# Kernel optimization log

Measured on AMD Instinct MI355X. Metric: run time of the kernel, lower is better.

The kernel has to match this reference:

```python
import jax, jax.numpy as jnp
import numpy as np


def setup_inputs() -> dict:
    key = jax.random.key(0)
    k1, k2, k3, k4, k5 = jax.random.split(key, 5)
    B, C, V, D, O = 8, 64, 25000, 12, 64
    x = jax.random.normal(k1, (B, C, V), dtype=jnp.float32)
    nbr_idx = jax.random.randint(k2, (B, V, D), 0, V, dtype=jnp.int32)
    # true 1-ring valence in [1, D]
    deg = jax.random.randint(k3, (B, V), 1, D + 1, dtype=jnp.int32)
    # conv weight [O, C, 1, 2] flattened to [O, C, 2], fan-in init scale
    W = jax.random.normal(k4, (O, C, 2), dtype=jnp.float32) * (1.0 / np.sqrt(C * 2))
    b = jax.random.normal(k5, (O,), dtype=jnp.float32) * 0.01
    return {"x": x, "nbr_idx": nbr_idx, "deg": deg, "W": W, "b": b}


def reference(x, nbr_idx, deg, W, b):
    # x: [B, C, V]; nbr_idx: [B, V, D] padded 1-ring; deg: [B, V] valid count
    B, C, V = x.shape
    D = nbr_idx.shape[-1]
    # gather neighbor features: [B, C, V, D]
    gathered = jax.vmap(lambda xb, ib: xb[:, ib])(x, nbr_idx)
    mask = (jnp.arange(D, dtype=deg.dtype)[None, None, :] < deg[:, :, None])  # [B, V, D]
    maskf = mask.astype(x.dtype)[:, None, :, :]  # [B, 1, V, D]
    denom = jnp.maximum(deg, 1).astype(x.dtype)[:, None, :]  # [B, 1, V]
    nbr_mean = jnp.sum(gathered * maskf, axis=-1) / denom  # [B, C, V]
    # G: [B, C, V, 2] = (self feature, 1-ring mean); conv2d kernel (1,2)
    G = jnp.stack([x, nbr_mean], axis=-1)
    out = jnp.einsum('bcvk,ock->bov', G, W) + b[None, :, None]
    return out[..., None]  # [B, O, V, 1]
```

## Files before the change

kernel.cpp:

```cpp
#include <hip/hip_runtime.h>
#include <stdint.h>


#define NB 8
#define NC 64
#define NV 25000
#define ND 12
#define NO 64
#define VT 98
#define GT 391

typedef uint32_t u32x4 __attribute__((ext_vector_type(4)));
typedef uint32_t u32x2 __attribute__((ext_vector_type(2)));
typedef __bf16  bf16x8 __attribute__((ext_vector_type(8)));
typedef float   f32x4  __attribute__((ext_vector_type(4)));

__device__ inline uint32_t bf16pack(float a, float b) {
    uint32_t ua = __float_as_uint(a), ub = __float_as_uint(b);
    ua = (ua + 0x7fffu + ((ua >> 16) & 1u)) >> 16;
    ub = (ub + 0x7fffu + ((ub >> 16) & 1u)) >> 16;
    return ua | (ub << 16);
}
__device__ inline float blo(uint32_t u) { return __uint_as_float(u << 16); }
__device__ inline float bhi(uint32_t u) { return __uint_as_float(u & 0xffff0000u); }

__global__ __launch_bounds__(256) void wt_kernel(const float* __restrict__ W,
                                                 uint32_t* __restrict__ Wcb) {
    int i = blockIdx.x * 256 + threadIdx.x;
    int m = i >> 5;
    int c = (i & 31) * 2;
    int k = m >> 6;
    int o = m & 63;
    float s0 = W[o * (NC * 2) + c * 2 + k];
    float s1 = W[o * (NC * 2) + (c + 1) * 2 + k];
    Wcb[i] = bf16pack(s0, s1);
}

__global__ __launch_bounds__(256) void ygemm_mfma(const float* __restrict__ x,
                                                  const uint32_t* __restrict__ Wcb,
                                                  const float* __restrict__ bias,
                                                  uint32_t* __restrict__ y0,
                                                  uint32_t* __restrict__ y1) {
    const int b = blockIdx.x & 7;
    const int tile = blockIdx.x >> 3;
    const int wave = threadIdx.x >> 6;
    const int lane = threadIdx.x & 63;
    const int l15 = lane & 15;
    const int lq = lane >> 4;
    const int v = tile * 64 + wave * 16 + l15;
    const int vc = v < NV ? v : NV - 1;
    const float* xb = x + (size_t)b * NC * NV;

    union BU { uint32_t u[4]; bf16x8 v; } bu[2];
#pragma unroll
    for (int kt = 0; kt < 2; ++kt) {
        const float* xc = xb + (size_t)(kt * 32 + lq * 8) * NV + vc;
#pragma unroll
        for (int jp = 0; jp < 4; ++jp) {
            float s0 = __builtin_nontemporal_load(xc + (size_t)(2 * jp) * NV);
            float s1 = __builtin_nontemporal_load(xc + (size_t)(2 * jp + 1) * NV);
            bu[kt].u[jp] = bf16pack(s0, s1);
        }
    }

    f32x4 acc[8];
#pragma unroll
    for (int mt = 0; mt < 8; ++mt) acc[mt] = (f32x4){0.f, 0.f, 0.f, 0.f};

#pragma unroll
    for (int mt = 0; mt < 8; ++mt) {
#pragma unroll
        for (int kt = 0; kt < 2; ++kt) {
            union { u32x4 q; bf16x8 v; } au;
            au.q = *(const u32x4*)(Wcb + (size_t)(mt * 16 + l15) * 32 + kt * 16 + lq * 4);
            acc[mt] = __builtin_amdgcn_mfma_f32_16x16x32_bf16(au.v, bu[kt].v, acc[mt], 0, 0, 0);
        }
    }

    if (v < NV) {
        uint32_t* yr0 = y0 + ((size_t)b * NV + v) * 32;
        uint32_t* yr1 = y1 + ((size_t)b * NV + v) * 32;
#pragma unroll
        for (int mt = 0; mt < 8; ++mt) {
            const int mo = mt * 16 + lq * 4;
            f32x4 a = acc[mt];
            if (mt < 4) {
                const float* bp = bias + mo;
                a[0] += bp[0]; a[1] += bp[1]; a[2] += bp[2]; a[3] += bp[3];
                u32x2 p = {bf16pack(a[0], a[1]), bf16pack(a[2], a[3])};
                __builtin_nontemporal_store(p, (u32x2*)(yr0 + (mo >> 1)));
            } else {
                u32x2 p = {bf16pack(a[0], a[1]), bf16pack(a[2], a[3])};
                *(u32x2*)(yr1 + ((mo - 64) >> 1)) = p;
            }
        }
    }
}

__global__ __launch_bounds__(256) void gather_out(const int* __restrict__ nbr,
                                                  const int* __restrict__ deg,
                                                  const uint32_t* __restrict__ y0,
                                                  const uint32_t* __restrict__ y1,
                                                  float* __restrict__ out) {
    const int b = blockIdx.x & 7;
    const int tile = blockIdx.x >> 3;
    const int v = tile * 256 + threadIdx.x;
    const int vc = v < NV ? v : NV - 1;
    const bool valid = (v < NV);
    const size_t bv = (size_t)b * NV + vc;

    int idxr[ND];
    {
        const int4* p = reinterpret_cast<const int4*>(nbr + bv * ND);
        int4 a0 = p[0], a1 = p[1], a2 = p[2];
        idxr[0] = a0.x; idxr[1] = a0.y; idxr[2]  = a0.z; idxr[3]  = a0.w;
        idxr[4] = a1.x; idxr[5] = a1.y; idxr[6]  = a1.z; idxr[7]  = a1.w;
        idxr[8] = a2.x; idxr[9] = a2.y; idxr[10] = a2.z; idxr[11] = a2.w;
    }
    const int dg = deg[bv];
    const float inv = 1.0f / (float)dg;
    const uint32_t* y1b = y1 + (size_t)b * NV * 32;

#pragma unroll 1
    for (int h = 0; h < 2; ++h) {
        float ns[32];
#pragma unroll
        for (int j = 0; j < 32; ++j) ns[j] = 0.0f;

#pragma unroll
        for (int d = 0; d < ND; ++d) {
            if (d < dg) {
                const u32x4* row =
                    reinterpret_cast<const u32x4*>(y1b + (size_t)idxr[d] * 32 + h * 16);
#pragma unroll
                for (int q = 0; q < 4; ++q) {
                    u32x4 u = row[q];
                    ns[q * 8 + 0] += blo(u[0]); ns[q * 8 + 1] += bhi(u[0]);
                    ns[q * 8 + 2] += blo(u[1]); ns[q * 8 + 3] += bhi(u[1]);
                    ns[q * 8 + 4] += blo(u[2]); ns[q * 8 + 5] += bhi(u[2]);
                    ns[q * 8 + 6] += blo(u[3]); ns[q * 8 + 7] += bhi(u[3]);
                }
            }
        }

        if (valid) {
            const u32x4* srow = reinterpret_cast<const u32x4*>(y0 + bv * 32 + h * 16);
#pragma unroll
            for (int q = 0; q < 4; ++q) {
                u32x4 u = __builtin_nontemporal_load(srow + q);
                float r[8];
                r[0] = blo(u[0]); r[1] = bhi(u[0]); r[2] = blo(u[1]); r[3] = bhi(u[1]);
                r[4] = blo(u[2]); r[5] = bhi(u[2]); r[6] = blo(u[3]); r[7] = bhi(u[3]);
#pragma unroll
                for (int t = 0; t < 8; ++t) {
                    float val = __builtin_fmaf(inv, ns[q * 8 + t], r[t]);
                    __builtin_nontemporal_store(
                        val, out + ((size_t)b * NO + h * 32 + q * 8 + t) * NV + v);
                }
            }
        }
    }
}

__global__ __launch_bounds__(64) void fallback_kernel(const float* __restrict__ x,
                                                      const int* __restrict__ nbr,
                                                      const int* __restrict__ deg,
                                                      const float* __restrict__ W,
                                                      const float* __restrict__ bias,
                                                      float* __restrict__ out) {
    const int bvi = blockIdx.x;
    const int b = bvi / NV, v = bvi % NV;
    const int o = threadIdx.x;
    const int degv = deg[bvi];
    const float inv = 1.0f / (float)degv;
    float acc = bias[o];
    for (int c = 0; c < NC; ++c) {
        const float* xc = x + ((size_t)b * NC + c) * NV;
        float m = 0.0f;
        for (int d = 0; d < degv; ++d) m += xc[nbr[(size_t)bvi * ND + d]];
        acc += W[o * (NC * 2) + c * 2] * xc[v] + W[o * (NC * 2) + c * 2 + 1] * (m * inv);
    }
    out[((size_t)b * NO + o) * NV + v] = acc;
}

extern "C" void kernel_launch(void* const* d_in, const int* in_sizes, int n_in,
                              void* d_out, int out_size, void* d_ws, size_t ws_size,
                              hipStream_t stream) {
    const float* x    = (const float*)d_in[0];
    const int*   nbr  = (const int*)d_in[1];
    const int*   deg  = (const int*)d_in[2];
    const float* W    = (const float*)d_in[3];
    const float* bias = (const float*)d_in[4];
    float* out = (float*)d_out;

    const size_t wcb_dw = 4096;
    const size_t yplane = (size_t)NB * NV * 32;
    const size_t need = (wcb_dw + 2 * yplane) * 4;
    if (ws_size >= need) {
        uint32_t* Wcb = (uint32_t*)d_ws;
        uint32_t* y0 = Wcb + wcb_dw;
        uint32_t* y1 = y0 + yplane;
        wt_kernel<<<dim3(16), 256, 0, stream>>>(W, Wcb);
        ygemm_mfma<<<dim3(NB * GT), 256, 0, stream>>>(x, Wcb, bias, y0, y1);
        gather_out<<<dim3(NB * VT), 256, 0, stream>>>(nbr, deg, y0, y1, out);
    } else {
        fallback_kernel<<<dim3(NB * NV), 64, 0, stream>>>(x, nbr, deg, W, bias, out);
    }
}
```

Measured before the change: 202.6 us.

## Split gather kernel across eight lanes per vertex with batched neighbor loads

The gather/output kernel now maps each vertex to eight lanes, each lane owning a 16-byte slice (8 output channels) of the bf16 y rows, instead of one thread looping over all 64 channels in two halves. All neighbor row loads are issued up front into registers before accumulation, and the grid grows eightfold. This raises parallelism and memory-level parallelism for the random row gathers and makes each neighbor row read contiguous across lanes. In exchange, neighbor indices and degree are loaded redundantly by eight lanes, and output stores become 32-byte runs per channel rather than full-wave contiguous runs.

```diff
diff --git a/kernel.cpp b/kernel.cpp
--- a/kernel.cpp
+++ b/kernel.cpp
@@ -7,8 +7,8 @@
 #define NV 25000
 #define ND 12
 #define NO 64
-#define VT 98
 #define GT 391
+#define GVT 782
 
 typedef uint32_t u32x4 __attribute__((ext_vector_type(4)));
 typedef uint32_t u32x2 __attribute__((ext_vector_type(2)));
@@ -104,7 +104,11 @@
                                                   float* __restrict__ out) {
     const int b = blockIdx.x & 7;
     const int tile = blockIdx.x >> 3;
-    const int v = tile * 256 + threadIdx.x;
+    const int lane = threadIdx.x & 63;
+    const int wave = threadIdx.x >> 6;
+    const int s = lane >> 3;
+    const int j = lane & 7;
+    const int v = tile * 32 + wave * 8 + s;
     const int vc = v < NV ? v : NV - 1;
     const bool valid = (v < NV);
     const size_t bv = (size_t)b * NV + vc;
@@ -121,43 +125,39 @@
     const float inv = 1.0f / (float)dg;
     const uint32_t* y1b = y1 + (size_t)b * NV * 32;
 
-#pragma unroll 1
-    for (int h = 0; h < 2; ++h) {
-        float ns[32];
-#pragma unroll
-        for (int j = 0; j < 32; ++j) ns[j] = 0.0f;
-
-#pragma unroll
-        for (int d = 0; d < ND; ++d) {
-            if (d < dg) {
-                const u32x4* row =
-                    reinterpret_cast<const u32x4*>(y1b + (size_t)idxr[d] * 32 + h * 16);
-#pragma unroll
-                for (int q = 0; q < 4; ++q) {
-                    u32x4 u = row[q];
-                    ns[q * 8 + 0] += blo(u[0]); ns[q * 8 + 1] += bhi(u[0]);
-                    ns[q * 8 + 2] += blo(u[1]); ns[q * 8 + 3] += bhi(u[1]);
-                    ns[q * 8 + 4] += blo(u[2]); ns[q * 8 + 5] += bhi(u[2]);
-                    ns[q * 8 + 6] += blo(u[3]); ns[q * 8 + 7] += bhi(u[3]);
-                }
-            }
-        }
-
-        if (valid) {
-            const u32x4* srow = reinterpret_cast<const u32x4*>(y0 + bv * 32 + h * 16);
-#pragma unroll
-            for (int q = 0; q < 4; ++q) {
-                u32x4 u = __builtin_nontemporal_load(srow + q);
-                float r[8];
-                r[0] = blo(u[0]); r[1] = bhi(u[0]); r[2] = blo(u[1]); r[3] = bhi(u[1]);
-                r[4] = blo(u[2]); r[5] = bhi(u[2]); r[6] = blo(u[3]); r[7] = bhi(u[3]);
-#pragma unroll
-                for (int t = 0; t < 8; ++t) {
-                    float val = __builtin_fmaf(inv, ns[q * 8 + t], r[t]);
-                    __builtin_nontemporal_store(
-                        val, out + ((size_t)b * NO + h * 32 + q * 8 + t) * NV + v);
-                }
-            }
+    u32x4 su = __builtin_nontemporal_load(
+        reinterpret_cast<const u32x4*>(y0 + bv * 32) + j);
+
+    u32x4 rows[ND];
+#pragma unroll
+    for (int d = 0; d < ND; ++d) {
+        if (d < dg)
+            rows[d] = *(reinterpret_cast<const u32x4*>(y1b + (size_t)idxr[d] * 32) + j);
+    }
+
+    float ns[8];
+#pragma unroll
+    for (int t = 0; t < 8; ++t) ns[t] = 0.0f;
+#pragma unroll
+    for (int d = 0; d < ND; ++d) {
+        if (d < dg) {
+            u32x4 u = rows[d];
+            ns[0] += blo(u[0]); ns[1] += bhi(u[0]);
+            ns[2] += blo(u[1]); ns[3] += bhi(u[1]);
+            ns[4] += blo(u[2]); ns[5] += bhi(u[2]);
+            ns[6] += blo(u[3]); ns[7] += bhi(u[3]);
+        }
+    }
+
+    if (valid) {
+        float r[8];
+        r[0] = blo(su[0]); r[1] = bhi(su[0]); r[2] = blo(su[1]); r[3] = bhi(su[1]);
+        r[4] = blo(su[2]); r[5] = bhi(su[2]); r[6] = blo(su[3]); r[7] = bhi(su[3]);
+#pragma unroll
+        for (int t = 0; t < 8; ++t) {
+            float val = __builtin_fmaf(inv, ns[t], r[t]);
+            __builtin_nontemporal_store(
+                val, out + ((size_t)b * NO + j * 8 + t) * NV + v);
         }
     }
 }
@@ -202,7 +202,7 @@
         uint32_t* y1 = y0 + yplane;
         wt_kernel<<<dim3(16), 256, 0, stream>>>(W, Wcb);
         ygemm_mfma<<<dim3(NB * GT), 256, 0, stream>>>(x, Wcb, bias, y0, y1);
-        gather_out<<<dim3(NB * VT), 256, 0, stream>>>(nbr, deg, y0, y1, out);
+        gather_out<<<dim3(NB * GVT), 256, 0, stream>>>(nbr, deg, y0, y1, out);
     } else {
         fallback_kernel<<<dim3(NB * NV), 64, 0, stream>>>(x, nbr, deg, W, bias, out);
     }
```

Result: no change. 204.5 us (+1.0%).
